# Performance work log

Measured on AMD Instinct MI355X. Metric: run time of the kernel, lower is better.

The kernel has to match this reference:

```python
import jax, jax.numpy as jnp
import numpy as np

B, L, Z, G = 512, 2713, 58, 8  # batch, chem features, seq len (zeta), d_model (gamma)
H, HD, FF, NL = 8, 1, 2048, 6  # heads, head_dim, ffn dim, layers
RNA_IN, LIN1, LIN2 = 1018, 256, 64
CAT, C1, C2 = LIN2 + Z * G, 64, 8  # 528, 64, 8


def setup_inputs() -> dict:
    key = jax.random.key(0)
    ks = iter(jax.random.split(key, 40))
    r = lambda shape, s=0.05: (jax.random.normal(next(ks), shape, dtype=jnp.float32) * s)
    inp = {
        'rna': jax.random.normal(next(ks), (B, RNA_IN), dtype=jnp.float32),
        'drug': jax.random.normal(next(ks), (B, L, Z), dtype=jnp.float32),
        'lin1_w': r((LIN1, RNA_IN)), 'lin1_b': r((LIN1,)),
        'lin2_w': r((LIN2, LIN1)), 'lin2_b': r((LIN2,)),
        'chem_w': r((G, L)),  # chem_embedding: Linear(2713->8, no bias)
        'pos_w': r((G, Z)),   # pos_embedding on one-hot == its weight columns
        'qkv_w': r((NL, 3 * G, G)), 'qkv_b': r((NL, 3 * G)),
        'out_w': r((NL, G, G)), 'out_b': r((NL, G)),
        'ln1_g': jnp.ones((NL, G), jnp.float32), 'ln1_b': jnp.zeros((NL, G), jnp.float32),
        'ff1_w': r((NL, FF, G)), 'ff1_b': r((NL, FF)),
        'ff2_w': r((NL, G, FF)), 'ff2_b': r((NL, G)),
        'ln2_g': jnp.ones((NL, G), jnp.float32), 'ln2_b': jnp.zeros((NL, G), jnp.float32),
        'c1_w': r((C1, CAT)), 'c1_b': r((C1,)),
        'c2_w': r((C2, C1)), 'c2_b': r((C2,)),
        'c3_w': r((1, C2)), 'c3_b': r((1,)),
    }
    return inp


def _layernorm(x, g, b, eps=1e-5):
    mu = jnp.mean(x, axis=-1, keepdims=True)
    var = jnp.mean(jnp.square(x - mu), axis=-1, keepdims=True)
    return (x - mu) * jax.lax.rsqrt(var + eps) * g + b


def _forward(rna, drug, lin1_w, lin1_b, lin2_w, lin2_b, chem_w, pos_w,
             qkv_w, qkv_b, out_w, out_b, ln1_g, ln1_b,
             ff1_w, ff1_b, ff2_w, ff2_b, ln2_g, ln2_b,
             c1_w, c1_b, c2_w, c2_b, c3_w, c3_b):
    # rna branch: two linear layers (no activation in original forward)
    r = rna @ lin1_w.T + lin1_b
    r = r @ lin2_w.T + lin2_b  # [B, 64]

    # Embedding: E = W_chem @ M + W_pos (the double loop, vectorized)
    E = jnp.einsum('gl,blz->bgz', chem_w, drug) + pos_w[None]  # [B, G, Z]
    x = jnp.transpose(E, (0, 2, 1))  # [B, Z, G] (batch_first transformer input)

    scale = 1.0 / np.sqrt(HD)
    for i in range(NL):  # 6 post-norm TransformerEncoderLayers, relu FFN
        qkv = x @ qkv_w[i].T + qkv_b[i]  # [B, Z, 3G]
        q, k, v = jnp.split(qkv, 3, axis=-1)
        qh = q.reshape(B, Z, H, HD)
        kh = k.reshape(B, Z, H, HD)
        vh = v.reshape(B, Z, H, HD)
        scores = jnp.einsum('bshd,bthd->bhst', qh, kh) * scale
        a = jax.nn.softmax(scores, axis=-1)
        o = jnp.einsum('bhst,bthd->bshd', a, vh).reshape(B, Z, G)
        o = o @ out_w[i].T + out_b[i]
        x = _layernorm(x + o, ln1_g[i], ln1_b[i])
        ff = jax.nn.relu(x @ ff1_w[i].T + ff1_b[i]) @ ff2_w[i].T + ff2_b[i]
        x = _layernorm(x + ff, ln2_g[i], ln2_b[i])

    flat = x.reshape(B, Z * G)  # [B, 464]
    h = jnp.concatenate([r, flat], axis=1)  # [B, 528]
    h = h @ c1_w.T + c1_b
    h = h @ c2_w.T + c2_b
    return h @ c3_w.T + c3_b  # [B, 1]


def reference(rna, drug, lin1_w, lin1_b, lin2_w, lin2_b, chem_w, pos_w,
              qkv_w, qkv_b, out_w, out_b, ln1_g, ln1_b,
              ff1_w, ff1_b, ff2_w, ff2_b, ln2_g, ln2_b,
              c1_w, c1_b, c2_w, c2_b, c3_w, c3_b):
    return _forward(rna, drug, lin1_w, lin1_b, lin2_w, lin2_b, chem_w, pos_w,
                    qkv_w, qkv_b, out_w, out_b, ln1_g, ln1_b,
                    ff1_w, ff1_b, ff2_w, ff2_b, ln2_g, ln2_b,
                    c1_w, c1_b, c2_w, c2_b, c3_w, c3_b)
```

## Files before the change

### kernel.cpp

```cpp
#include <hip/hip_runtime.h>

#define BB 512
#define LDIM 2713
#define ZDIM 58
#define GDIM 8
#define NLAYER 6
#define FFDIM 2048
#define RNAIN 1018
#define CATDIM 528
#define NCAT 1482

typedef float v2f __attribute__((ext_vector_type(2)));
typedef float f32x4 __attribute__((ext_vector_type(4)));
typedef _Float16 f16x4 __attribute__((ext_vector_type(4)));

#define OFF_CWT    0
#define OFF_TMATT  21704
#define OFF_BR     38088
#define OFF_WCATT  38152
#define OFF_BPRIME 133000
#define OFF_W1H    133064
#define OFF_A2H    182216

__global__ void prep0_kernel(const float* __restrict__ chem_w,
                             const float* __restrict__ ff1_w, const float* __restrict__ ff2_w,
                             const float* __restrict__ c1_w, const float* __restrict__ lin2_w,
                             const float* __restrict__ lin1_b, const float* __restrict__ lin2_b,
                             float* __restrict__ ws) {
    int tid = blockIdx.x * 256 + threadIdx.x;
    float* cwT   = ws + OFF_CWT;
    float* TmatT = ws + OFF_TMATT;
    float* bR    = ws + OFF_BR;
    _Float16* w1hp = (_Float16*)(ws + OFF_W1H);
    _Float16* a2hp = (_Float16*)(ws + OFF_A2H);

    if (tid < 21704) {
        int l = tid >> 3, g = tid & 7;
        cwT[tid] = chem_w[g * LDIM + l];
        return;
    }
    int r1 = tid - 21704;
    if (r1 < NLAYER * 128 * 32) {
        int li = r1 / 4096, rem = r1 % 4096;
        int ft = rem >> 5, l32 = rem & 31;
        int q = l32 >> 4, i = l32 & 15;
        const float* src = ff1_w + ((size_t)li * FFDIM + ft * 16 + i) * 8 + q * 4;
        size_t dst = ((size_t)(li * 128 + ft) * 32 + l32) * 4;
        #pragma unroll
        for (int j = 0; j < 4; ++j) w1hp[dst + j] = (_Float16)src[j];
        return;
    }
    int r2 = r1 - NLAYER * 128 * 32;
    if (r2 < NLAYER * 128 * 32) {
        int li = r2 / 4096, rem = r2 % 4096;
        int ft = rem >> 5, s = rem & 31;
        int q = s >> 3, i2 = s & 7;
        const float* src = ff2_w + ((size_t)li * GDIM + i2) * FFDIM + ft * 16 + q * 4;
        size_t dst = ((size_t)(li * 128 + ft) * 32 + s) * 4;
        #pragma unroll
        for (int j = 0; j < 4; ++j) a2hp[dst + j] = (_Float16)src[j];
        return;
    }
    int r3 = r2 - NLAYER * 128 * 32;
    if (r3 < 256 * 64) {
        int n = r3 >> 6, j = r3 & 63;
        float a = 0.f;
        for (int m = 0; m < 64; ++m) a += c1_w[j * CATDIM + m] * lin2_w[m * 256 + n];
        TmatT[r3] = a;
        return;
    }
    int r4 = r3 - 256 * 64;
    if (r4 < 64) {
        float a = lin2_b[r4];
        for (int n = 0; n < 256; ++n) a += lin2_w[r4 * 256 + n] * lin1_b[n];
        bR[r4] = a;
    }
}

__global__ void prep1_kernel(const float* __restrict__ lin1_w, const float* __restrict__ c1_w,
                             const float* __restrict__ c1_b, const float* __restrict__ ws_in,
                             float* __restrict__ ws) {
    int tid = blockIdx.x * 256 + threadIdx.x;
    const float* TmatT = ws_in + OFF_TMATT;
    const float* bR    = ws_in + OFF_BR;
    float* WcatT  = ws + OFF_WCATT;
    float* bprime = ws + OFF_BPRIME;
    if (tid < RNAIN * 64) {
        int k = tid >> 6, j = tid & 63;
        float a = 0.f;
        #pragma unroll 4
        for (int n = 0; n < 256; ++n) a += TmatT[n * 64 + j] * lin1_w[n * RNAIN + k];
        WcatT[tid] = a;
        return;
    }
    int q = tid - RNAIN * 64;
    if (q < 464 * 64) {
        int kk = q >> 6, j = q & 63;
        WcatT[(RNAIN + kk) * 64 + j] = c1_w[j * CATDIM + 64 + kk];
        return;
    }
    int j = q - 464 * 64;
    if (j < 64) {
        float a = c1_b[j];
        for (int m = 0; m < 64; ++m) a += c1_w[j * CATDIM + m] * bR[m];
        bprime[j] = a;
    }
}

__global__ __launch_bounds__(1024, 4) void main_kernel(
    const float* __restrict__ drug, const float* __restrict__ pos_w,
    const float* __restrict__ cwT,
    const _Float16* __restrict__ w1h, const _Float16* __restrict__ a2h,
    const float* __restrict__ ff1_b,
    const float* __restrict__ qkv_w, const float* __restrict__ qkv_b,
    const float* __restrict__ out_w, const float* __restrict__ out_b,
    const float* __restrict__ ln1_g, const float* __restrict__ ln1_b,
    const float* __restrict__ ff2_b,
    const float* __restrict__ ln2_g, const float* __restrict__ ln2_b,
    const float* __restrict__ rna, const float* __restrict__ WcatT,
    const float* __restrict__ bprime,
    const float* __restrict__ c2_w, const float* __restrict__ c2_b,
    const float* __restrict__ c3_w, const float* __restrict__ c3_b,
    float* __restrict__ out) {
    __shared__ float smem[12712];
    float* xs    = smem;
    float* qs    = smem + 512;
    float* ks    = smem + 992;
    float* vs    = smem + 1472;
    float* os    = smem + 1952;
    float* part  = smem + 2464;
    float* qkvws = smem + 10656;
    float* qkvbs = smem + 11808;
    float* outws = smem + 11952;
    float* outbs = smem + 12336;
    float* l1gs  = smem + 12384;
    float* l1bs  = smem + 12432;
    float* l2gs  = smem + 12480;
    float* l2bs  = smem + 12528;
    float* f2bs  = smem + 12576;
    float* h1s   = smem + 12624;
    float* h2s   = smem + 12688;

    const int b = blockIdx.x;
    const int t = threadIdx.x;
    const int w = __builtin_amdgcn_readfirstlane(t >> 6);
    const int lane = t & 63;
    const int quad = lane >> 4;
    const int i16 = lane & 15;

    for (int i = t; i < 1152; i += 1024) qkvws[i] = qkv_w[i];
    if (t < 144) qkvbs[t] = qkv_b[t];
    if (t < 384) outws[t] = out_w[t];
    if (t < 48) {
        outbs[t] = out_b[t];
        l1gs[t] = ln1_g[t]; l1bs[t] = ln1_b[t];
        l2gs[t] = ln2_g[t]; l2bs[t] = ln2_b[t];
        f2bs[t] = ff2_b[t];
    }

    {
        int z = (lane < ZDIM) ? lane : (ZDIM - 1);
        const float* dp = drug + (size_t)b * (LDIM * ZDIM);
        v2f a0 = {0.f, 0.f}, a1 = {0.f, 0.f}, a2 = {0.f, 0.f}, a3 = {0.f, 0.f};
        int l0 = w * 170;
        int l1 = (l0 + 170 < LDIM) ? (l0 + 170) : LDIM;
        int l = l0;
        for (; l + 8 <= l1; l += 8) {
            float d[8];
            #pragma unroll
            for (int ii = 0; ii < 8; ++ii) d[ii] = dp[(l + ii) * ZDIM + z];
            #pragma unroll
            for (int ii = 0; ii < 8; ++ii) {
                const v2f* cw = (const v2f*)(cwT + (l + ii) * 8);
                v2f dd = {d[ii], d[ii]};
                a0 += cw[0] * dd; a1 += cw[1] * dd; a2 += cw[2] * dd; a3 += cw[3] * dd;
            }
        }
        for (; l < l1; ++l) {
            float d = dp[l * ZDIM + z];
            const v2f* cw = (const v2f*)(cwT + l * 8);
            v2f dd = {d, d};
            a0 += cw[0] * dd; a1 += cw[1] * dd; a2 += cw[2] * dd; a3 += cw[3] * dd;
        }
        v2f* pr = (v2f*)(part + (w * 64 + lane) * 8);
        pr[0] = a0; pr[1] = a1; pr[2] = a2; pr[3] = a3;
    }
    __syncthreads();
    if (t < 512) {
        if (t < 464) {
            int z = t >> 3, g = t & 7;
            float s = 0.f;
            #pragma unroll
            for (int ww = 0; ww < 16; ++ww) s += part[(ww * 64 + z) * 8 + g];
            xs[t] = s + pos_w[g * ZDIM + z];
        } else {
            xs[t] = 0.f;
        }
    }
    __syncthreads();

    for (int li = 0; li < NLAYER; ++li) {
        if (t < 464) {
            int z = t >> 3, h = t & 7;
            const float4* xr = (const float4*)(xs + z * 8);
            float4 x0 = xr[0], x1 = xr[1];
            #pragma unroll
            for (int p = 0; p < 3; ++p) {
                int j = p * 8 + h;
                const float4* wr = (const float4*)(qkvws + li * 192 + j * 8);
                float4 w0 = wr[0], w1 = wr[1];
                float a = qkvbs[li * 24 + j]
                        + x0.x * w0.x + x0.y * w0.y + x0.z * w0.z + x0.w * w0.w
                        + x1.x * w1.x + x1.y * w1.y + x1.z * w1.z + x1.w * w1.w;
                float* dst = (p == 0) ? qs : (p == 1) ? ks : vs;
                dst[h * 60 + z] = a;
            }
        }
        __syncthreads();

        if (t < 464) {
            int h = t & 7, s = t >> 3;
            float q = qs[h * 60 + s];
            const float4* kr = (const float4*)(ks + h * 60);
            const float4* vr = (const float4*)(vs + h * 60);
            float sum = 0.f, oa = 0.f;
            #pragma unroll 2
            for (int c = 0; c < 14; ++c) {
                float4 k4 = kr[c], v4 = vr[c];
                float e0 = __expf(q * k4.x); sum += e0; oa += e0 * v4.x;
                float e1 = __expf(q * k4.y); sum += e1; oa += e1 * v4.y;
                float e2 = __expf(q * k4.z); sum += e2; oa += e2 * v4.z;
                float e3 = __expf(q * k4.w); sum += e3; oa += e3 * v4.w;
            }
            {
                const float* kk = ks + h * 60;
                const float* vv = vs + h * 60;
                float e0 = __expf(q * kk[56]); sum += e0; oa += e0 * vv[56];
                float e1 = __expf(q * kk[57]); sum += e1; oa += e1 * vv[57];
            }
            os[t] = oa / sum;
        }
        __syncthreads();

        if (t < 464) {
            int z = t >> 3, g = t & 7;
            const float4* orow = (const float4*)(os + z * 8);
            float4 o0 = orow[0], o1 = orow[1];
            const float4* wr = (const float4*)(outws + li * 64 + g * 8);
            float4 w0 = wr[0], w1 = wr[1];
            float a = outbs[li * 8 + g] + xs[t]
                    + o0.x * w0.x + o0.y * w0.y + o0.z * w0.z + o0.w * w0.w
                    + o1.x * w1.x + o1.y * w1.y + o1.z * w1.z + o1.w * w1.w;
            float s8 = a + __shfl_xor(a, 1);
            s8 += __shfl_xor(s8, 2);
            s8 += __shfl_xor(s8, 4);
            float mu = s8 * 0.125f;
            float d = a - mu;
            float vv = d * d;
            vv += __shfl_xor(vv, 1); vv += __shfl_xor(vv, 2); vv += __shfl_xor(vv, 4);
            float inv = rsqrtf(vv * 0.125f + 1e-5f);
            xs[t] = d * inv * l1gs[li * 8 + g] + l1bs[li * 8 + g];
        }
        __syncthreads();

        {
            f16x4 xb[4];
            #pragma unroll
            for (int nt = 0; nt < 4; ++nt) {
                if (quad < 2) {
                    const float4* xp = (const float4*)(xs + (nt * 16 + i16) * 8 + quad * 4);
                    float4 xv = *xp;
                    xb[nt][0] = (_Float16)xv.x; xb[nt][1] = (_Float16)xv.y;
                    xb[nt][2] = (_Float16)xv.z; xb[nt][3] = (_Float16)xv.w;
                } else {
                    xb[nt][0] = (_Float16)0.f; xb[nt][1] = (_Float16)0.f;
                    xb[nt][2] = (_Float16)0.f; xb[nt][3] = (_Float16)0.f;
                }
            }
            f32x4 oacc[4];
            #pragma unroll
            for (int nt = 0; nt < 4; ++nt) { oacc[nt][0]=0.f; oacc[nt][1]=0.f; oacc[nt][2]=0.f; oacc[nt][3]=0.f; }

            const _Float16* w1p = w1h + ((size_t)(li * 128 + w * 8) * 32) * 4;
            const _Float16* a2p = a2h + ((size_t)(li * 128 + w * 8) * 32) * 4;
            const float* b1p = ff1_b + li * FFDIM + w * 128;

            #pragma unroll 2
            for (int ft = 0; ft < 8; ++ft) {
                f16x4 w1f = {};
                if (lane < 32) w1f = *(const f16x4*)(w1p + (size_t)(ft * 32 + lane) * 4);
                f16x4 a2f = {};
                if (i16 < 8) a2f = *(const f16x4*)(a2p + (size_t)(ft * 32 + quad * 8 + i16) * 4);
                f32x4 b1v = *(const f32x4*)(b1p + ft * 16 + quad * 4);
                #pragma unroll
                for (int nt = 0; nt < 4; ++nt) {
                    f32x4 h = b1v;
                    h = __builtin_amdgcn_mfma_f32_16x16x16f16(w1f, xb[nt], h, 0, 0, 0);
                    h[0] = fmaxf(h[0], 0.f); h[1] = fmaxf(h[1], 0.f);
                    h[2] = fmaxf(h[2], 0.f); h[3] = fmaxf(h[3], 0.f);
                    f16x4 hb;
                    hb[0] = (_Float16)h[0]; hb[1] = (_Float16)h[1];
                    hb[2] = (_Float16)h[2]; hb[3] = (_Float16)h[3];
                    oacc[nt] = __builtin_amdgcn_mfma_f32_16x16x16f16(a2f, hb, oacc[nt], 0, 0, 0);
                }
            }
            if (quad < 2) {
                #pragma unroll
                for (int nt = 0; nt < 4; ++nt) {
                    float4 o4 = make_float4(oacc[nt][0], oacc[nt][1], oacc[nt][2], oacc[nt][3]);
                    *(float4*)(part + ((w * 64 + nt * 16 + i16) * 8 + quad * 4)) = o4;
                }
            }
        }
        __syncthreads();

        if (t < 464) {
            int z = t >> 3, g = t & 7;
            float s = 0.f;
            #pragma unroll
            for (int ww = 0; ww < 16; ++ww) s += part[(ww * 64 + z) * 8 + g];
            float a = xs[t] + s + f2bs[li * 8 + g];
            float s8 = a + __shfl_xor(a, 1);
            s8 += __shfl_xor(s8, 2);
            s8 += __shfl_xor(s8, 4);
            float mu = s8 * 0.125f;
            float d = a - mu;
            float vv = d * d;
            vv += __shfl_xor(vv, 1); vv += __shfl_xor(vv, 2); vv += __shfl_xor(vv, 4);
            float inv = rsqrtf(vv * 0.125f + 1e-5f);
            xs[t] = d * inv * l2gs[li * 8 + g] + l2bs[li * 8 + g];
        }
        __syncthreads();
    }

    {
        float* cat = part;
        float* partial = part + 4096;
        const float* rg = rna + (size_t)b * RNAIN;
        for (int i = t; i < RNAIN; i += 1024) cat[i] = rg[i];
        __syncthreads();
        int j = lane;
        int k0 = w * 93;
        int k1 = (k0 + 93 < NCAT) ? (k0 + 93) : NCAT;
        float a = (w == 0) ? bprime[j] : 0.f;
        #pragma unroll 4
        for (int k = k0; k < k1; ++k) {
            float ck = (k < RNAIN) ? cat[k] : xs[k - RNAIN];
            a += ck * WcatT[k * 64 + j];
        }
        partial[w * 64 + j] = a;
        __syncthreads();
        if (t < 64) {
            float s = 0.f;
            #pragma unroll
            for (int ww = 0; ww < 16; ++ww) s += partial[ww * 64 + t];
            h1s[t] = s;
        }
    }
    __syncthreads();
    if (t < 8) {
        float a2 = c2_b[t];
        #pragma unroll 8
        for (int m = 0; m < 64; ++m) a2 += h1s[m] * c2_w[t * 64 + m];
        h2s[t] = a2;
    }
    __syncthreads();
    if (t == 0) {
        float a3 = c3_b[0];
        #pragma unroll
        for (int jj = 0; jj < 8; ++jj) a3 += h2s[jj] * c3_w[jj];
        out[b] = a3;
    }
}

extern "C" void kernel_launch(void* const* d_in, const int* in_sizes, int n_in,
                              void* d_out, int out_size, void* d_ws, size_t ws_size,
                              hipStream_t stream) {
    const float* rna    = (const float*)d_in[0];
    const float* drug   = (const float*)d_in[1];
    const float* lin1_w = (const float*)d_in[2];
    const float* lin1_b = (const float*)d_in[3];
    const float* lin2_w = (const float*)d_in[4];
    const float* lin2_b = (const float*)d_in[5];
    const float* chem_w = (const float*)d_in[6];
    const float* pos_w  = (const float*)d_in[7];
    const float* qkv_w  = (const float*)d_in[8];
    const float* qkv_b  = (const float*)d_in[9];
    const float* out_w  = (const float*)d_in[10];
    const float* out_b  = (const float*)d_in[11];
    const float* ln1_g  = (const float*)d_in[12];
    const float* ln1_b  = (const float*)d_in[13];
    const float* ff1_w  = (const float*)d_in[14];
    const float* ff1_b  = (const float*)d_in[15];
    const float* ff2_w  = (const float*)d_in[16];
    const float* ff2_b  = (const float*)d_in[17];
    const float* ln2_g  = (const float*)d_in[18];
    const float* ln2_b  = (const float*)d_in[19];
    const float* c1_w   = (const float*)d_in[20];
    const float* c1_b   = (const float*)d_in[21];
    const float* c2_w   = (const float*)d_in[22];
    const float* c2_b   = (const float*)d_in[23];
    const float* c3_w   = (const float*)d_in[24];
    const float* c3_b   = (const float*)d_in[25];
    float* ws  = (float*)d_ws;
    float* out = (float*)d_out;

    const float* cwT      = ws + OFF_CWT;
    const _Float16* w1h   = (const _Float16*)(ws + OFF_W1H);
    const _Float16* a2h   = (const _Float16*)(ws + OFF_A2H);
    const float* WcatT    = ws + OFF_WCATT;
    const float* bprime   = ws + OFF_BPRIME;

    hipLaunchKernelGGL(prep0_kernel, dim3(342), dim3(256), 0, stream,
                       chem_w, ff1_w, ff2_w, c1_w, lin2_w, lin1_b, lin2_b, ws);
    hipLaunchKernelGGL(prep1_kernel, dim3(371), dim3(256), 0, stream,
                       lin1_w, c1_w, c1_b, ws, ws);
    hipLaunchKernelGGL(main_kernel, dim3(BB), dim3(1024), 0, stream,
                       drug, pos_w, cwT, w1h, a2h, ff1_b,
                       qkv_w, qkv_b, out_w, out_b,
                       ln1_g, ln1_b, ff2_b, ln2_g, ln2_b,
                       rna, WcatT, bprime, c2_w, c2_b, c3_w, c3_b, out);
}
```

Baseline: 622.0 us.

## Split drug embedding into separate multi-block kernel with LDS-staged chem weights

Moves the large drug×chem_w embedding reduction out of the main transformer kernel into a dedicated kernel that splits the L dimension into four chunks per batch (2048 blocks), staging the chem weight slice in shared memory and writing partial sums to workspace. The main kernel then sums the four partials plus the positional term. This is meant to spread the memory-bound read of the drug tensor over many more workgroups and to shorten the main kernel. It adds an extra launch and a workspace round-trip, and raises main_kernel's launch_bounds occupancy hint.

Result: faster. 609.5 us (-2.0%).

```diff
diff --git a/kernel.cpp b/kernel.cpp
--- a/kernel.cpp
+++ b/kernel.cpp
@@ -9,37 +9,97 @@
 #define RNAIN 1018
 #define CATDIM 528
 #define NCAT 1482
+#define LQ 679
 
 typedef float v2f __attribute__((ext_vector_type(2)));
 typedef float f32x4 __attribute__((ext_vector_type(4)));
 typedef _Float16 f16x4 __attribute__((ext_vector_type(4)));
 
-#define OFF_CWT    0
-#define OFF_TMATT  21704
-#define OFF_BR     38088
-#define OFF_WCATT  38152
-#define OFF_BPRIME 133000
-#define OFF_W1H    133064
-#define OFF_A2H    182216
-
-__global__ void prep0_kernel(const float* __restrict__ chem_w,
-                             const float* __restrict__ ff1_w, const float* __restrict__ ff2_w,
+#define OFF_TMATT  0
+#define OFF_BR     16384
+#define OFF_WCATT  16448
+#define OFF_BPRIME 111296
+#define OFF_W1H    111360
+#define OFF_A2H    160512
+#define OFF_EPART  209664
+
+__global__ __launch_bounds__(512, 8) void embed_kernel(
+    const float* __restrict__ drug, const float* __restrict__ chem_w,
+    float* __restrict__ epart) {
+    __shared__ float cwl[LQ * 8 + 8];
+    __shared__ float part[8][ZDIM][8];
+    const int bq = blockIdx.x;
+    const int b = bq >> 2, q = bq & 3;
+    const int t = threadIdx.x;
+    const int w = t >> 6;
+    const int lane = t & 63;
+    const int l0 = q * LQ;
+    const int nrows = (LDIM - l0 < LQ) ? (LDIM - l0) : LQ;
+
+    #pragma unroll
+    for (int g = 0; g < 8; ++g)
+        for (int i = t; i < nrows; i += 512)
+            cwl[i * 8 + g] = chem_w[g * LDIM + l0 + i];
+    __syncthreads();
+
+    {
+        int z = (lane < ZDIM) ? lane : (ZDIM - 1);
+        const float* dp = drug + (size_t)b * (LDIM * ZDIM) + (size_t)l0 * ZDIM;
+        v2f a0 = {0.f, 0.f}, a1 = {0.f, 0.f}, a2 = {0.f, 0.f}, a3 = {0.f, 0.f};
+        int r0 = w * 85;
+        int r1 = (r0 + 85 < nrows) ? (r0 + 85) : nrows;
+        int r = r0;
+        for (; r + 4 <= r1; r += 4) {
+            float d0 = dp[(r + 0) * ZDIM + z];
+            float d1 = dp[(r + 1) * ZDIM + z];
+            float d2 = dp[(r + 2) * ZDIM + z];
+            float d3 = dp[(r + 3) * ZDIM + z];
+            const v2f* c0 = (const v2f*)(cwl + (r + 0) * 8);
+            const v2f* c1 = (const v2f*)(cwl + (r + 1) * 8);
+            const v2f* c2 = (const v2f*)(cwl + (r + 2) * 8);
+            const v2f* c3 = (const v2f*)(cwl + (r + 3) * 8);
+            v2f dd;
+            dd = (v2f){d0, d0};
+            a0 += c0[0] * dd; a1 += c0[1] * dd; a2 += c0[2] * dd; a3 += c0[3] * dd;
+            dd = (v2f){d1, d1};
+            a0 += c1[0] * dd; a1 += c1[1] * dd; a2 += c1[2] * dd; a3 += c1[3] * dd;
+            dd = (v2f){d2, d2};
+            a0 += c2[0] * dd; a1 += c2[1] * dd; a2 += c2[2] * dd; a3 += c2[3] * dd;
+            dd = (v2f){d3, d3};
+            a0 += c3[0] * dd; a1 += c3[1] * dd; a2 += c3[2] * dd; a3 += c3[3] * dd;
+        }
+        for (; r < r1; ++r) {
+            float d = dp[r * ZDIM + z];
+            const v2f* cc = (const v2f*)(cwl + r * 8);
+            v2f dd = {d, d};
+            a0 += cc[0] * dd; a1 += cc[1] * dd; a2 += cc[2] * dd; a3 += cc[3] * dd;
+        }
+        if (lane < ZDIM) {
+            v2f* pr = (v2f*)(&part[w][z][0]);
+            pr[0] = a0; pr[1] = a1; pr[2] = a2; pr[3] = a3;
+        }
+    }
+    __syncthreads();
+    if (t < 464) {
+        int z = t >> 3, g = t & 7;
+        float s = 0.f;
+        #pragma unroll
+        for (int ww = 0; ww < 8; ++ww) s += part[ww][z][g];
+        epart[(size_t)bq * 464 + t] = s;
+    }
+}
+
+__global__ void prep0_kernel(const float* __restrict__ ff1_w, const float* __restrict__ ff2_w,
                              const float* __restrict__ c1_w, const float* __restrict__ lin2_w,
                              const float* __restrict__ lin1_b, const float* __restrict__ lin2_b,
                              float* __restrict__ ws) {
     int tid = blockIdx.x * 256 + threadIdx.x;
-    float* cwT   = ws + OFF_CWT;
     float* TmatT = ws + OFF_TMATT;
     float* bR    = ws + OFF_BR;
     _Float16* w1hp = (_Float16*)(ws + OFF_W1H);
     _Float16* a2hp = (_Float16*)(ws + OFF_A2H);
 
-    if (tid < 21704) {
-        int l = tid >> 3, g = tid & 7;
-        cwT[tid] = chem_w[g * LDIM + l];
-        return;
-    }
-    int r1 = tid - 21704;
+    int r1 = tid;
     if (r1 < NLAYER * 128 * 32) {
         int li = r1 / 4096, rem = r1 % 4096;
         int ft = rem >> 5, l32 = rem & 31;
@@ -78,11 +138,10 @@
 }
 
 __global__ void prep1_kernel(const float* __restrict__ lin1_w, const float* __restrict__ c1_w,
-                             const float* __restrict__ c1_b, const float* __restrict__ ws_in,
-                             float* __restrict__ ws) {
+                             const float* __restrict__ c1_b, float* __restrict__ ws) {
     int tid = blockIdx.x * 256 + threadIdx.x;
-    const float* TmatT = ws_in + OFF_TMATT;
-    const float* bR    = ws_in + OFF_BR;
+    const float* TmatT = ws + OFF_TMATT;
+    const float* bR    = ws + OFF_BR;
     float* WcatT  = ws + OFF_WCATT;
     float* bprime = ws + OFF_BPRIME;
     if (tid < RNAIN * 64) {
@@ -107,9 +166,8 @@
     }
 }
 
-__global__ __launch_bounds__(1024, 4) void main_kernel(
-    const float* __restrict__ drug, const float* __restrict__ pos_w,
-    const float* __restrict__ cwT,
+__global__ __launch_bounds__(1024, 8) void main_kernel(
+    const float* __restrict__ epart, const float* __restrict__ pos_w,
     const _Float16* __restrict__ w1h, const _Float16* __restrict__ a2h,
     const float* __restrict__ ff1_b,
     const float* __restrict__ qkv_w, const float* __restrict__ qkv_b,
@@ -158,41 +216,12 @@
         f2bs[t] = ff2_b[t];
     }
 
-    {
-        int z = (lane < ZDIM) ? lane : (ZDIM - 1);
-        const float* dp = drug + (size_t)b * (LDIM * ZDIM);
-        v2f a0 = {0.f, 0.f}, a1 = {0.f, 0.f}, a2 = {0.f, 0.f}, a3 = {0.f, 0.f};
-        int l0 = w * 170;
-        int l1 = (l0 + 170 < LDIM) ? (l0 + 170) : LDIM;
-        int l = l0;
-        for (; l + 8 <= l1; l += 8) {
-            float d[8];
-            #pragma unroll
-            for (int ii = 0; ii < 8; ++ii) d[ii] = dp[(l + ii) * ZDIM + z];
-            #pragma unroll
-            for (int ii = 0; ii < 8; ++ii) {
-                const v2f* cw = (const v2f*)(cwT + (l + ii) * 8);
-                v2f dd = {d[ii], d[ii]};
-                a0 += cw[0] * dd; a1 += cw[1] * dd; a2 += cw[2] * dd; a3 += cw[3] * dd;
-            }
-        }
-        for (; l < l1; ++l) {
-            float d = dp[l * ZDIM + z];
-            const v2f* cw = (const v2f*)(cwT + l * 8);
-            v2f dd = {d, d};
-            a0 += cw[0] * dd; a1 += cw[1] * dd; a2 += cw[2] * dd; a3 += cw[3] * dd;
-        }
-        v2f* pr = (v2f*)(part + (w * 64 + lane) * 8);
-        pr[0] = a0; pr[1] = a1; pr[2] = a2; pr[3] = a3;
-    }
-    __syncthreads();
     if (t < 512) {
         if (t < 464) {
             int z = t >> 3, g = t & 7;
-            float s = 0.f;
-            #pragma unroll
-            for (int ww = 0; ww < 16; ++ww) s += part[(ww * 64 + z) * 8 + g];
-            xs[t] = s + pos_w[g * ZDIM + z];
+            const float* ep = epart + (size_t)(b * 4) * 464 + t;
+            float s = ep[0] + ep[464] + ep[928] + ep[1392] + pos_w[g * ZDIM + z];
+            xs[t] = s;
         } else {
             xs[t] = 0.f;
         }
@@ -405,18 +434,20 @@
     float* ws  = (float*)d_ws;
     float* out = (float*)d_out;
 
-    const float* cwT      = ws + OFF_CWT;
+    float* epart          = ws + OFF_EPART;
     const _Float16* w1h   = (const _Float16*)(ws + OFF_W1H);
     const _Float16* a2h   = (const _Float16*)(ws + OFF_A2H);
     const float* WcatT    = ws + OFF_WCATT;
     const float* bprime   = ws + OFF_BPRIME;
 
-    hipLaunchKernelGGL(prep0_kernel, dim3(342), dim3(256), 0, stream,
-                       chem_w, ff1_w, ff2_w, c1_w, lin2_w, lin1_b, lin2_b, ws);
+    hipLaunchKernelGGL(embed_kernel, dim3(BB * 4), dim3(512), 0, stream,
+                       drug, chem_w, epart);
+    hipLaunchKernelGGL(prep0_kernel, dim3(257), dim3(256), 0, stream,
+                       ff1_w, ff2_w, c1_w, lin2_w, lin1_b, lin2_b, ws);
     hipLaunchKernelGGL(prep1_kernel, dim3(371), dim3(256), 0, stream,
-                       lin1_w, c1_w, c1_b, ws, ws);
+                       lin1_w, c1_w, c1_b, ws);
     hipLaunchKernelGGL(main_kernel, dim3(BB), dim3(1024), 0, stream,
-                       drug, pos_w, cwT, w1h, a2h, ff1_b,
+                       epart, pos_w, w1h, a2h, ff1_b,
                        qkv_w, qkv_b, out_w, out_b,
                        ln1_g, ln1_b, ff2_b, ln2_g, ln2_b,
                        rna, WcatT, bprime, c2_w, c2_b, c3_w, c3_b, out);
```
